# Kernel optimization log

Hardware: AMD Instinct MI355X
Metric: run time of the kernel (lower is better)

Reference implementation:

```python
import jax, jax.numpy as jnp
import numpy as np


def _dct2(x):
    """DCT-II over last dim, scipy norm=None scaling (matches the torch rfft trick:
    X_k = 2 * sum_n x_n cos(pi*k*(2n+1)/(2N))). Expressed as one batched matmul."""
    N = x.shape[-1]
    n = jnp.arange(N, dtype=x.dtype)
    k = jnp.arange(N, dtype=x.dtype)
    # D[k, n] = 2*cos(pi*k*(2n+1)/(2N))
    D = 2.0 * jnp.cos((np.pi / (2.0 * N)) * k[:, None] * (2.0 * n[None, :] + 1.0))
    return jnp.einsum('kn,bcn->bck', D, x)


def setup_inputs() -> dict:
    key = jax.random.key(0)
    k0, k1, k2 = jax.random.split(key, 3)
    b, c, l = 32, 512, 1024
    x = jax.random.normal(k0, (b, c, l), dtype=jnp.float32)
    # 1x1 Conv1d weights (kernel_size=1, bias=False) stored as [out, in]
    w1 = jax.random.normal(k1, (2 * c, c), dtype=jnp.float32) / np.float32(np.sqrt(c))
    w2 = jax.random.normal(k2, (c, 2 * c), dtype=jnp.float32) / np.float32(np.sqrt(2 * c))
    ln_w = jnp.ones((l,), dtype=jnp.float32)
    ln_b = jnp.zeros((l,), dtype=jnp.float32)
    return {"x": x, "w1": w1, "w2": w2, "ln_w": ln_w, "ln_b": ln_b}


def reference(x, w1, w2, ln_w, ln_b):
    eps = 1e-6
    freq = _dct2(x)                                   # [b, c, l]
    mu = jnp.mean(freq, axis=-1, keepdims=True)
    var = jnp.var(freq, axis=-1, keepdims=True)       # biased, like nn.LayerNorm
    h = (freq - mu) * jax.lax.rsqrt(var + eps) * ln_w + ln_b
    # fc: Conv1d(c->2c, k=1) -> Dropout(eval: identity) -> ReLU -> Conv1d(2c->c) -> Sigmoid
    h = jax.nn.relu(jnp.einsum('oi,bil->bol', w1, h))  # [b, 2c, l]
    gate = jax.nn.sigmoid(jnp.einsum('oi,bil->bol', w2, h))  # [b, c, l]
    return x * gate
```

## Files before the change

kernel.cpp:

```cpp
#include <hip/hip_runtime.h>
#include <hip/hip_bf16.h>
#include <math.h>

typedef short short8 __attribute__((ext_vector_type(8)));
typedef short short4v __attribute__((ext_vector_type(4)));
typedef float f32x4 __attribute__((ext_vector_type(4)));

__device__ __forceinline__ short f2bf(float f) {
  union { float f; unsigned u; } v; v.f = f;
  unsigned r = v.u + 0x7FFFu + ((v.u >> 16) & 1u);
  return (short)(r >> 16);
}
__device__ __forceinline__ float bf2f(short s) {
  union { unsigned u; float f; } v; v.u = ((unsigned)(unsigned short)s) << 16;
  return v.f;
}

__global__ __launch_bounds__(256) void cast_kernel(const float* __restrict__ in,
                                                   short* __restrict__ out, int n4) {
  int i = blockIdx.x * blockDim.x + threadIdx.x;
  if (i < n4) {
    float4 v = ((const float4*)in)[i];
    short4v o;
    o.x = f2bf(v.x); o.y = f2bf(v.y); o.z = f2bf(v.z); o.w = f2bf(v.w);
    ((short4v*)out)[i] = o;
  }
}

__global__ __launch_bounds__(256) void prep_eo(const float* __restrict__ x,
                                               short* __restrict__ eo) {
  int t = blockIdx.x * 256 + threadIdx.x;
  int bc = t >> 7, n0 = (t & 127) * 4;
  const float* xr = x + (size_t)bc * 1024;
  float4 f = *(const float4*)(xr + n0);
  float4 r = *(const float4*)(xr + 1020 - n0);
  short4v ef, of;
  ef.x = f2bf(f.x + r.w); ef.y = f2bf(f.y + r.z); ef.z = f2bf(f.z + r.y); ef.w = f2bf(f.w + r.x);
  of.x = f2bf(f.x - r.w); of.y = f2bf(f.y - r.z); of.z = f2bf(f.z - r.y); of.w = f2bf(f.w - r.x);
  *(short4v*)&eo[(size_t)bc * 512 + n0] = ef;
  *(short4v*)&eo[8388608 + (size_t)bc * 512 + n0] = of;
}

__global__ __launch_bounds__(256) void build_Deo(short* __restrict__ D) {
  int t = blockIdx.x * 256 + threadIdx.x;
  int parity = t >> 18, rem = t & 262143;
  int k2 = rem >> 9, n = rem & 511;
  const float s = 1.5339807878856412e-03f;
  float arg = (s * (float)(2 * k2 + parity)) * (float)(2 * n + 1);
  D[t] = f2bf(2.0f * cosf(arg));
}

__global__ __launch_bounds__(256) void ln_stats(const float2* __restrict__ partial,
                                                float2* __restrict__ musd) {
  int n = blockIdx.x * 256 + threadIdx.x;
  float S = 0.f, Q = 0.f;
#pragma unroll
  for (int r = 0; r < 4; ++r) {
    float2 p = partial[(size_t)r * 16384 + n];
    S += p.x; Q += p.y;
  }
  float mu  = S * (1.f / 1024.f);
  float var = Q * (1.f / 1024.f) - mu * mu;
  float2 o; o.x = mu; o.y = rsqrtf(var + 1e-6f);
  musd[n] = o;
}

__global__ __launch_bounds__(256) void ln_apply(short* __restrict__ freqT,
                                                const float2* __restrict__ musd,
                                                const float* __restrict__ lnw,
                                                const float* __restrict__ lnb) {
  int t = blockIdx.x * 256 + threadIdx.x;
  int c8 = t & 63;
  int k  = (t >> 6) & 1023;
  int b  = t >> 16;
  size_t idx = ((size_t)b << 19) + (size_t)k * 512 + (size_t)c8 * 8;
  short8 v = *(const short8*)&freqT[idx];
  float w  = lnw[k];
  float bb = lnb[k];
  const float2* ms = &musd[b * 512 + c8 * 8];
  short8 o;
#pragma unroll
  for (int j = 0; j < 8; ++j) {
    float f = bf2f(v[j]);
    float2 m = ms[j];
    o[j] = f2bf((f - m.x) * m.y * w + bb);
  }
  *(short8*)&freqT[idx] = o;
}

template<int EPI>
__global__ __launch_bounds__(256, 2) void gemmF(
    const short* __restrict__ A, const short* __restrict__ B,
    void* __restrict__ Cout, const float* __restrict__ X,
    float2* __restrict__ P, int K, int NT, long strideA, long strideB)
{
  __shared__ short As[2][8192];
  __shared__ short Bs[2][4096];
  const int tid = threadIdx.x;
  const int l   = tid & 63;
  const int w   = tid >> 6;
  const int wm  = w >> 1;
  const int wc  = w & 1;
  const int lr  = l & 15;
  const int lhi = l >> 4;

  const int nwg = gridDim.x, q = nwg >> 3, orig = blockIdx.x;
  const int wgid = (orig & 7) * q + (orig >> 3);
  int bx, by, bz;
  bx = wgid & 1; bz = (wgid >> 1) & 1; by = wgid >> 2;

  const long row0 = (long)bx * 256, col0 = (long)by * 128;
  const short* Ab = A + (size_t)bz * strideA + (size_t)row0 * K;
  const short* Bb = B + (size_t)bz * strideB + (size_t)col0 * K;

  const int sx    = (lhi ^ ((lr >> 1) & 3)) * 8;
  const int abase = (wm * 128 + lr) * 32;
  const int bbase = (wc * 64  + lr) * 32;

  f32x4 acc[8][4];
#pragma unroll
  for (int i = 0; i < 8; ++i)
#pragma unroll
    for (int j = 0; j < 4; ++j) acc[i][j] = (f32x4){0.f, 0.f, 0.f, 0.f};

#define GLL(SRC, DST) __builtin_amdgcn_global_load_lds(                      \
      (const __attribute__((address_space(1))) void*)(SRC),                  \
      (__attribute__((address_space(3))) void*)(DST), 16, 0, 0)

#define STAGE(KT, D) do {                                                    \
    const size_t kb_ = (size_t)(KT) * 32;                                    \
    _Pragma("unroll")                                                        \
    for (int r_ = 0; r_ < 4; ++r_) {                                         \
      int c_ = r_ * 256 + tid; int row_ = c_ >> 2; int sl_ = c_ & 3;         \
      int sc_ = (sl_ ^ ((row_ >> 1) & 3)) * 8;                               \
      GLL(Ab + (size_t)row_ * K + kb_ + sc_, &As[D][row_ * 32 + sl_ * 8]);   \
    }                                                                        \
    _Pragma("unroll")                                                        \
    for (int r_ = 0; r_ < 2; ++r_) {                                         \
      int c_ = r_ * 256 + tid; int row_ = c_ >> 2; int sl_ = c_ & 3;         \
      int sc_ = (sl_ ^ ((row_ >> 1) & 3)) * 8;                               \
      GLL(Bb + (size_t)row_ * K + kb_ + sc_, &Bs[D][row_ * 32 + sl_ * 8]);   \
    }                                                                        \
  } while (0)

#define LD8(PTR, OFF) (*(const short8*)&(PTR)[OFF])
#define MFMA(AV, BV, C) __builtin_amdgcn_mfma_f32_16x16x32_bf16(AV, BV, C, 0, 0, 0)
#define SBAR __builtin_amdgcn_s_barrier()
#define SCHB __builtin_amdgcn_sched_barrier(0)

#define MROW(MI, AV)                                                         \
    acc[MI][0] = MFMA(AV, b0, acc[MI][0]);                                   \
    acc[MI][1] = MFMA(AV, b1, acc[MI][1]);                                   \
    acc[MI][2] = MFMA(AV, b2, acc[MI][2]);                                   \
    acc[MI][3] = MFMA(AV, b3, acc[MI][3]);

  STAGE(0, 0);
  STAGE(1, 1);

  int cur = 0;
  for (int kt = 0; kt < NT; ++kt) {
    if (kt + 1 < NT) { asm volatile("s_waitcnt vmcnt(6)" ::: "memory"); }
    else             { asm volatile("s_waitcnt vmcnt(0)" ::: "memory"); }
    SCHB; SBAR;
    const short* Ad = As[cur];
    const short* Bd = Bs[cur];
    short8 a0, a1, a2, a3, a4, a5, a6, a7, b0, b1, b2, b3;
    a0 = LD8(Ad, abase + 0 * 512 + sx);
    a1 = LD8(Ad, abase + 1 * 512 + sx);
    b0 = LD8(Bd, bbase + 0 * 512 + sx);
    b1 = LD8(Bd, bbase + 1 * 512 + sx);
    b2 = LD8(Bd, bbase + 2 * 512 + sx);
    b3 = LD8(Bd, bbase + 3 * 512 + sx);
    a2 = LD8(Ad, abase + 2 * 512 + sx);
    a3 = LD8(Ad, abase + 3 * 512 + sx);
    a4 = LD8(Ad, abase + 4 * 512 + sx);
    a5 = LD8(Ad, abase + 5 * 512 + sx);
    a6 = LD8(Ad, abase + 6 * 512 + sx);
    a7 = LD8(Ad, abase + 7 * 512 + sx);
    SCHB;
    asm volatile("s_waitcnt lgkmcnt(6)" ::: "memory");
    SCHB;
    __builtin_amdgcn_s_setprio(1);
    MROW(0, a0) MROW(1, a1)
    __builtin_amdgcn_s_setprio(0);
    SCHB;
    asm volatile("s_waitcnt lgkmcnt(0)" ::: "memory");
    SCHB; SBAR;
    if (kt + 2 < NT) STAGE(kt + 2, cur);
    SCHB;
    __builtin_amdgcn_s_setprio(1);
    MROW(2, a2) MROW(3, a3) MROW(4, a4) MROW(5, a5) MROW(6, a6) MROW(7, a7)
    __builtin_amdgcn_s_setprio(0);
    SCHB;
    cur ^= 1;
  }

  float sv[4], qv[4];
#pragma unroll
  for (int ni = 0; ni < 4; ++ni) { sv[ni] = 0.f; qv[ni] = 0.f; }

#pragma unroll
  for (int mi = 0; mi < 8; ++mi) {
#pragma unroll
    for (int ni = 0; ni < 4; ++ni) {
#pragma unroll
      for (int j = 0; j < 4; ++j) {
        int r  = (int)row0 + wm * 128 + mi * 16 + lhi * 4 + j;
        int cc = (int)col0 + wc * 64 + ni * 16 + lr;
        float v = acc[mi][ni][j];
        sv[ni] += v; qv[ni] += v * v;
        int rr = r * 2 + bz;
        ((short*)Cout)[((size_t)(cc >> 9) << 19) + (size_t)rr * 512 + (cc & 511)] = f2bf(v);
      }
    }
  }

  {
    __syncthreads();
    float* redS = (float*)&As[0][0];
    float* redQ = redS + 1024;
    const int contrib = wm * 4 + lhi;
#pragma unroll
    for (int ni = 0; ni < 4; ++ni) {
      int ccl = wc * 64 + ni * 16 + lr;
      redS[ccl * 8 + contrib] = sv[ni];
      redQ[ccl * 8 + contrib] = qv[ni];
    }
    __syncthreads();
    if (tid < 128) {
      float S = 0.f, Q = 0.f;
#pragma unroll
      for (int i = 0; i < 8; ++i) { S += redS[tid * 8 + i]; Q += redQ[tid * 8 + i]; }
      float2 o; o.x = S; o.y = Q;
      P[(size_t)(bz * 2 + bx) * 16384 + col0 + tid] = o;
    }
  }
#undef MROW
#undef MFMA
#undef LD8
#undef STAGE
#undef GLL
#undef SBAR
#undef SCHB
}

template<int EPI>
__global__ __launch_bounds__(256, 2) void gemm128(
    const short* __restrict__ A, const short* __restrict__ B,
    void* __restrict__ Cout, const float* __restrict__ X,
    int K, int NT, long strideA, long strideB)
{
  __shared__ short As[2][8192];
  __shared__ short Bs[2][8192];
  const int tid = threadIdx.x;
  const int l   = tid & 63;
  const int w   = tid >> 6;
  const int wm  = w >> 1;
  const int wc  = w & 1;
  const int l7  = l & 7;
  const int lr  = l & 15;
  const int lhi = l >> 4;

  const int nwg = gridDim.x, q = nwg >> 3, orig = blockIdx.x;
  const int wgid = (orig & 7) * q + (orig >> 3);
  int bx, by, bz;
  if (EPI == 1) { by = wgid & 7; bx = (wgid >> 3) & 7; bz = wgid >> 6; }
  else          { bx = wgid & 3; by = (wgid >> 2) & 7; bz = wgid >> 5; }

  const long row0 = (long)bx * 128, col0 = (long)by * 128;
  const short* Ab = A + (size_t)bz * strideA + (size_t)row0 * K;
  const short* Bb = B + (size_t)bz * strideB + (size_t)col0 * K;

  const int rowb  = tid >> 3;
  const int colel = ((tid & 7) ^ ((tid >> 3) & 7)) * 8;
  const int abase = (wm * 64 + lr) * 64;
  const int bbase = (wc * 64 + lr) * 64;
  const int s0 = ((lhi    ) ^ l7) * 8;
  const int s1 = ((lhi + 4) ^ l7) * 8;

  f32x4 acc[4][4];
#pragma unroll
  for (int i = 0; i < 4; ++i)
#pragma unroll
    for (int j = 0; j < 4; ++j) acc[i][j] = (f32x4){0.f, 0.f, 0.f, 0.f};

#define GLL(SRC, DST) __builtin_amdgcn_global_load_lds(                      \
      (const __attribute__((address_space(1))) void*)(SRC),                  \
      (__attribute__((address_space(3))) void*)(DST), 16, 0, 0)

#define STAGE(KT, D) do {                                                    \
    const size_t ko_ = (size_t)(KT) * 64 + colel;                            \
    _Pragma("unroll")                                                        \
    for (int r_ = 0; r_ < 4; ++r_)                                           \
      GLL(Ab + (size_t)(r_ * 32 + rowb) * K + ko_,                           \
          &As[D][(r_ * 32 + rowb) * 64 + (tid & 7) * 8]);                    \
    _Pragma("unroll")                                                        \
    for (int r_ = 0; r_ < 4; ++r_)                                           \
      GLL(Bb + (size_t)(r_ * 32 + rowb) * K + ko_,                           \
          &Bs[D][(r_ * 32 + rowb) * 64 + (tid & 7) * 8]);                    \
  } while (0)

#define LD8(PTR, OFF) (*(const short8*)&(PTR)[OFF])
#define MFMA(AV, BV, C) __builtin_amdgcn_mfma_f32_16x16x32_bf16(AV, BV, C, 0, 0, 0)
#define SBAR __builtin_amdgcn_s_barrier()
#define SCHB __builtin_amdgcn_sched_barrier(0)

#define MFMA16(A0, A1, A2, A3, B0, B1, B2, B3)                               \
    __builtin_amdgcn_s_setprio(1);                                           \
    acc[0][0]=MFMA(A0,B0,acc[0][0]); acc[0][1]=MFMA(A0,B1,acc[0][1]);        \
    acc[0][2]=MFMA(A0,B2,acc[0][2]); acc[0][3]=MFMA(A0,B3,acc[0][3]);        \
    acc[1][0]=MFMA(A1,B0,acc[1][0]); acc[1][1]=MFMA(A1,B1,acc[1][1]);        \
    acc[1][2]=MFMA(A1,B2,acc[1][2]); acc[1][3]=MFMA(A1,B3,acc[1][3]);        \
    acc[2][0]=MFMA(A2,B0,acc[2][0]); acc[2][1]=MFMA(A2,B1,acc[2][1]);        \
    acc[2][2]=MFMA(A2,B2,acc[2][2]); acc[2][3]=MFMA(A2,B3,acc[2][3]);        \
    acc[3][0]=MFMA(A3,B0,acc[3][0]); acc[3][1]=MFMA(A3,B1,acc[3][1]);        \
    acc[3][2]=MFMA(A3,B2,acc[3][2]); acc[3][3]=MFMA(A3,B3,acc[3][3]);        \
    __builtin_amdgcn_s_setprio(0);

  STAGE(0, 0);
  STAGE(1, 1);

  int cur = 0;
  for (int kt = 0; kt < NT; ++kt) {
    if (kt + 1 < NT) { asm volatile("s_waitcnt vmcnt(8)" ::: "memory"); }
    else             { asm volatile("s_waitcnt vmcnt(0)" ::: "memory"); }
    SCHB; SBAR;
    const short* Ad = As[cur];
    const short* Bd = Bs[cur];
    short8 a00, a01, a02, a03, b00, b01, b02, b03;
    short8 a10, a11, a12, a13, b10, b11, b12, b13;
    a00 = LD8(Ad, abase + 0 * 1024 + s0);
    a01 = LD8(Ad, abase + 1 * 1024 + s0);
    a02 = LD8(Ad, abase + 2 * 1024 + s0);
    a03 = LD8(Ad, abase + 3 * 1024 + s0);
    b00 = LD8(Bd, bbase + 0 * 1024 + s0);
    b01 = LD8(Bd, bbase + 1 * 1024 + s0);
    b02 = LD8(Bd, bbase + 2 * 1024 + s0);
    b03 = LD8(Bd, bbase + 3 * 1024 + s0);
    a10 = LD8(Ad, abase + 0 * 1024 + s1);
    a11 = LD8(Ad, abase + 1 * 1024 + s1);
    a12 = LD8(Ad, abase + 2 * 1024 + s1);
    a13 = LD8(Ad, abase + 3 * 1024 + s1);
    b10 = LD8(Bd, bbase + 0 * 1024 + s1);
    b11 = LD8(Bd, bbase + 1 * 1024 + s1);
    b12 = LD8(Bd, bbase + 2 * 1024 + s1);
    b13 = LD8(Bd, bbase + 3 * 1024 + s1);
    SCHB;
    asm volatile("s_waitcnt lgkmcnt(8)" ::: "memory");
    SCHB;
    MFMA16(a00, a01, a02, a03, b00, b01, b02, b03)
    SCHB;
    asm volatile("s_waitcnt lgkmcnt(0)" ::: "memory");
    SCHB; SBAR;
    if (kt + 2 < NT) STAGE(kt + 2, cur);
    SCHB;
    MFMA16(a10, a11, a12, a13, b10, b11, b12, b13)
    SCHB;
    cur ^= 1;
  }

#pragma unroll
  for (int mi = 0; mi < 4; ++mi) {
#pragma unroll
    for (int ni = 0; ni < 4; ++ni) {
#pragma unroll
      for (int j = 0; j < 4; ++j) {
        int r  = (int)row0 + wm * 64 + mi * 16 + lhi * 4 + j;
        int cc = (int)col0 + wc * 64 + ni * 16 + lr;
        float v = acc[mi][ni][j];
        if (EPI == 1) {
          ((short*)Cout)[(size_t)bz * 1048576 + (size_t)r * 1024 + cc] = f2bf(v > 0.f ? v : 0.f);
        } else {
          size_t idx = (size_t)bz * 524288 + (size_t)r * 1024 + cc;
          float g = 1.f / (1.f + __expf(-v));
          ((float*)Cout)[idx] = X[idx] * g;
        }
      }
    }
  }
#undef MFMA16
#undef MFMA
#undef LD8
#undef STAGE
#undef GLL
#undef SBAR
#undef SCHB
}

extern "C" void kernel_launch(void* const* d_in, const int* in_sizes, int n_in,
                              void* d_out, int out_size, void* d_ws, size_t ws_size,
                              hipStream_t stream) {
  const float* x    = (const float*)d_in[0];
  const float* w1   = (const float*)d_in[1];
  const float* w2   = (const float*)d_in[2];
  const float* ln_w = (const float*)d_in[3];
  const float* ln_b = (const float*)d_in[4];
  float* out = (float*)d_out;

  char* ws = (char*)d_ws;
  short* Deo    = (short*)(ws);
  short* w1_bf  = (short*)(ws + 1048576);
  short* w2_bf  = (short*)(ws + 2097152);
  short* freqT  = (short*)(ws + 3145728);
  short* z1t    = (short*)(ws + 36700160);
  short* eo     = z1t;
  float2* part  = (float2*)(ws + 103809024);
  float2* musd  = (float2*)(ws + 104857600);

  prep_eo<<<dim3(8192), dim3(256), 0, stream>>>(x, eo);
  cast_kernel<<<dim3(512), dim3(256), 0, stream>>>(w1, w1_bf, 524288 / 4);
  cast_kernel<<<dim3(512), dim3(256), 0, stream>>>(w2, w2_bf, 524288 / 4);
  build_Deo<<<dim3(2048), dim3(256), 0, stream>>>(Deo);

  gemmF<0><<<dim3(512), dim3(256), 0, stream>>>(
      Deo, eo, (void*)freqT, nullptr, part, 512, 16, 262144, 8388608);

  ln_stats<<<dim3(64), dim3(256), 0, stream>>>(part, musd);

  ln_apply<<<dim3(8192), dim3(256), 0, stream>>>(freqT, musd, ln_w, ln_b);

  gemm128<1><<<dim3(2048), dim3(256), 0, stream>>>(
      freqT, w1_bf, (void*)z1t, nullptr, 512, 8, 524288, 0);

  gemm128<2><<<dim3(1024), dim3(256), 0, stream>>>(
      w2_bf, z1t, (void*)out, x, 1024, 16, 0, 1048576);
}
```

Before: 156.7 us.

## Halve gemm128 K-tile to 32 and raise occupancy to four blocks per CU

The K-step of the two FC GEMM kernels drops from 64 to 32. That halves the LDS buffers and the per-iteration register fragments, and launch bounds move from 2 to 4 workgroups per CU. The LDS swizzle is rebuilt for the 32-wide rows, and the MFMA issue is split into four rows with staggered lgkmcnt waits so compute can start before all LDS reads land. The cost is twice as many loop iterations, and so twice as many barriers and wait points per tile, in exchange for more wavefronts to hide latency.

```diff
diff --git a/kernel.cpp b/kernel.cpp
--- a/kernel.cpp
+++ b/kernel.cpp
@@ -245,19 +245,18 @@
 }
 
 template<int EPI>
-__global__ __launch_bounds__(256, 2) void gemm128(
+__global__ __launch_bounds__(256, 4) void gemm128(
     const short* __restrict__ A, const short* __restrict__ B,
     void* __restrict__ Cout, const float* __restrict__ X,
     int K, int NT, long strideA, long strideB)
 {
-  __shared__ short As[2][8192];
-  __shared__ short Bs[2][8192];
+  __shared__ short As[2][4096];
+  __shared__ short Bs[2][4096];
   const int tid = threadIdx.x;
   const int l   = tid & 63;
   const int w   = tid >> 6;
   const int wm  = w >> 1;
   const int wc  = w & 1;
-  const int l7  = l & 7;
   const int lr  = l & 15;
   const int lhi = l >> 4;
 
@@ -271,12 +270,9 @@
   const short* Ab = A + (size_t)bz * strideA + (size_t)row0 * K;
   const short* Bb = B + (size_t)bz * strideB + (size_t)col0 * K;
 
-  const int rowb  = tid >> 3;
-  const int colel = ((tid & 7) ^ ((tid >> 3) & 7)) * 8;
-  const int abase = (wm * 64 + lr) * 64;
-  const int bbase = (wc * 64 + lr) * 64;
-  const int s0 = ((lhi    ) ^ l7) * 8;
-  const int s1 = ((lhi + 4) ^ l7) * 8;
+  const int sx    = (lhi ^ ((lr >> 1) & 3)) * 8;
+  const int abase = (wm * 64 + lr) * 32;
+  const int bbase = (wc * 64 + lr) * 32;
 
   f32x4 acc[4][4];
 #pragma unroll
@@ -289,15 +285,19 @@
       (__attribute__((address_space(3))) void*)(DST), 16, 0, 0)
 
 #define STAGE(KT, D) do {                                                    \
-    const size_t ko_ = (size_t)(KT) * 64 + colel;                            \
+    const size_t kb_ = (size_t)(KT) * 32;                                    \
     _Pragma("unroll")                                                        \
-    for (int r_ = 0; r_ < 4; ++r_)                                           \
-      GLL(Ab + (size_t)(r_ * 32 + rowb) * K + ko_,                           \
-          &As[D][(r_ * 32 + rowb) * 64 + (tid & 7) * 8]);                    \
+    for (int r_ = 0; r_ < 2; ++r_) {                                         \
+      int c_ = r_ * 256 + tid; int row_ = c_ >> 2; int sl_ = c_ & 3;         \
+      int sc_ = (sl_ ^ ((row_ >> 1) & 3)) * 8;                               \
+      GLL(Ab + (size_t)row_ * K + kb_ + sc_, &As[D][row_ * 32 + sl_ * 8]);   \
+    }                                                                        \
     _Pragma("unroll")                                                        \
-    for (int r_ = 0; r_ < 4; ++r_)                                           \
-      GLL(Bb + (size_t)(r_ * 32 + rowb) * K + ko_,                           \
-          &Bs[D][(r_ * 32 + rowb) * 64 + (tid & 7) * 8]);                    \
+    for (int r_ = 0; r_ < 2; ++r_) {                                         \
+      int c_ = r_ * 256 + tid; int row_ = c_ >> 2; int sl_ = c_ & 3;         \
+      int sc_ = (sl_ ^ ((row_ >> 1) & 3)) * 8;                               \
+      GLL(Bb + (size_t)row_ * K + kb_ + sc_, &Bs[D][row_ * 32 + sl_ * 8]);   \
+    }                                                                        \
   } while (0)
 
 #define LD8(PTR, OFF) (*(const short8*)&(PTR)[OFF])
@@ -305,56 +305,57 @@
 #define SBAR __builtin_amdgcn_s_barrier()
 #define SCHB __builtin_amdgcn_sched_barrier(0)
 
-#define MFMA16(A0, A1, A2, A3, B0, B1, B2, B3)                               \
-    __builtin_amdgcn_s_setprio(1);                                           \
-    acc[0][0]=MFMA(A0,B0,acc[0][0]); acc[0][1]=MFMA(A0,B1,acc[0][1]);        \
-    acc[0][2]=MFMA(A0,B2,acc[0][2]); acc[0][3]=MFMA(A0,B3,acc[0][3]);        \
-    acc[1][0]=MFMA(A1,B0,acc[1][0]); acc[1][1]=MFMA(A1,B1,acc[1][1]);        \
-    acc[1][2]=MFMA(A1,B2,acc[1][2]); acc[1][3]=MFMA(A1,B3,acc[1][3]);        \
-    acc[2][0]=MFMA(A2,B0,acc[2][0]); acc[2][1]=MFMA(A2,B1,acc[2][1]);        \
-    acc[2][2]=MFMA(A2,B2,acc[2][2]); acc[2][3]=MFMA(A2,B3,acc[2][3]);        \
-    acc[3][0]=MFMA(A3,B0,acc[3][0]); acc[3][1]=MFMA(A3,B1,acc[3][1]);        \
-    acc[3][2]=MFMA(A3,B2,acc[3][2]); acc[3][3]=MFMA(A3,B3,acc[3][3]);        \
-    __builtin_amdgcn_s_setprio(0);
+#define MROW(MI, AV)                                                         \
+    acc[MI][0] = MFMA(AV, b0, acc[MI][0]);                                   \
+    acc[MI][1] = MFMA(AV, b1, acc[MI][1]);                                   \
+    acc[MI][2] = MFMA(AV, b2, acc[MI][2]);                                   \
+    acc[MI][3] = MFMA(AV, b3, acc[MI][3]);
 
   STAGE(0, 0);
   STAGE(1, 1);
 
   int cur = 0;
   for (int kt = 0; kt < NT; ++kt) {
-    if (kt + 1 < NT) { asm volatile("s_waitcnt vmcnt(8)" ::: "memory"); }
+    if (kt + 1 < NT) { asm volatile("s_waitcnt vmcnt(4)" ::: "memory"); }
     else             { asm volatile("s_waitcnt vmcnt(0)" ::: "memory"); }
     SCHB; SBAR;
     const short* Ad = As[cur];
     const short* Bd = Bs[cur];
-    short8 a00, a01, a02, a03, b00, b01, b02, b03;
-    short8 a10, a11, a12, a13, b10, b11, b12, b13;
-    a00 = LD8(Ad, abase + 0 * 1024 + s0);
-    a01 = LD8(Ad, abase + 1 * 1024 + s0);
-    a02 = LD8(Ad, abase + 2 * 1024 + s0);
-    a03 = LD8(Ad, abase + 3 * 1024 + s0);
-    b00 = LD8(Bd, bbase + 0 * 1024 + s0);
-    b01 = LD8(Bd, bbase + 1 * 1024 + s0);
-    b02 = LD8(Bd, bbase + 2 * 1024 + s0);
-    b03 = LD8(Bd, bbase + 3 * 1024 + s0);
-    a10 = LD8(Ad, abase + 0 * 1024 + s1);
-    a11 = LD8(Ad, abase + 1 * 1024 + s1);
-    a12 = LD8(Ad, abase + 2 * 1024 + s1);
-    a13 = LD8(Ad, abase + 3 * 1024 + s1);
-    b10 = LD8(Bd, bbase + 0 * 1024 + s1);
-    b11 = LD8(Bd, bbase + 1 * 1024 + s1);
-    b12 = LD8(Bd, bbase + 2 * 1024 + s1);
-    b13 = LD8(Bd, bbase + 3 * 1024 + s1);
-    SCHB;
-    asm volatile("s_waitcnt lgkmcnt(8)" ::: "memory");
-    SCHB;
-    MFMA16(a00, a01, a02, a03, b00, b01, b02, b03)
+    short8 a0, a1, a2, a3, b0, b1, b2, b3;
+    a0 = LD8(Ad, abase + 0 * 512 + sx);
+    b0 = LD8(Bd, bbase + 0 * 512 + sx);
+    b1 = LD8(Bd, bbase + 1 * 512 + sx);
+    b2 = LD8(Bd, bbase + 2 * 512 + sx);
+    b3 = LD8(Bd, bbase + 3 * 512 + sx);
+    a1 = LD8(Ad, abase + 1 * 512 + sx);
+    a2 = LD8(Ad, abase + 2 * 512 + sx);
+    a3 = LD8(Ad, abase + 3 * 512 + sx);
+    SCHB;
+    asm volatile("s_waitcnt lgkmcnt(3)" ::: "memory");
+    SCHB;
+    __builtin_amdgcn_s_setprio(1);
+    MROW(0, a0)
+    __builtin_amdgcn_s_setprio(0);
+    SCHB;
+    asm volatile("s_waitcnt lgkmcnt(2)" ::: "memory");
+    SCHB;
+    __builtin_amdgcn_s_setprio(1);
+    MROW(1, a1)
+    __builtin_amdgcn_s_setprio(0);
+    SCHB;
+    asm volatile("s_waitcnt lgkmcnt(1)" ::: "memory");
+    SCHB;
+    __builtin_amdgcn_s_setprio(1);
+    MROW(2, a2)
+    __builtin_amdgcn_s_setprio(0);
     SCHB;
     asm volatile("s_waitcnt lgkmcnt(0)" ::: "memory");
     SCHB; SBAR;
     if (kt + 2 < NT) STAGE(kt + 2, cur);
     SCHB;
-    MFMA16(a10, a11, a12, a13, b10, b11, b12, b13)
+    __builtin_amdgcn_s_setprio(1);
+    MROW(3, a3)
+    __builtin_amdgcn_s_setprio(0);
     SCHB;
     cur ^= 1;
   }
@@ -378,7 +379,7 @@
       }
     }
   }
-#undef MFMA16
+#undef MROW
 #undef MFMA
 #undef LD8
 #undef STAGE
@@ -420,8 +421,8 @@
   ln_apply<<<dim3(8192), dim3(256), 0, stream>>>(freqT, musd, ln_w, ln_b);
 
   gemm128<1><<<dim3(2048), dim3(256), 0, stream>>>(
-      freqT, w1_bf, (void*)z1t, nullptr, 512, 8, 524288, 0);
+      freqT, w1_bf, (void*)z1t, nullptr, 512, 16, 524288, 0);
 
   gemm128<2><<<dim3(1024), dim3(256), 0, stream>>>(
-      w2_bf, z1t, (void*)out, x, 1024, 16, 0, 1048576);
-}
+      w2_bf, z1t, (void*)out, x, 1024, 32, 0, 1048576);
+}
```

Measured after the change: 165.0 us. +5.3%, slower.
